# Performance work log

Hardware: AMD Instinct MI355X
Metric: run time of the kernel (lower is better)

The kernel has to match this reference:

```python
import jax, jax.numpy as jnp
import numpy as np

N_LIG, N_TGT, E = 100000, 20000, 1000000
H = 128

def setup_inputs() -> dict:
    key = jax.random.key(0)
    ks = jax.random.split(key, 20)
    def lin(k, fan_in, fan_out):
        k1, k2 = jax.random.split(k)
        lim = 1.0 / np.sqrt(fan_in)
        W = jax.random.uniform(k1, (fan_in, fan_out), jnp.float32, -lim, lim)
        b = jax.random.uniform(k2, (fan_out,), jnp.float32, -lim, lim)
        return W, b
    W_lig, b_lig = lin(ks[0], 4, H)
    W_tgt, b_tgt = lin(ks[1], 1280, H)
    W1f, b1f = lin(ks[2], H, H)   # conv1 ligand->target
    W1r, b1r = lin(ks[3], H, H)   # conv1 target->ligand
    W2f, b2f = lin(ks[4], H, H)   # conv2 ligand->target
    W2r, b2r = lin(ks[5], H, H)   # conv2 target->ligand
    Wp1, bp1 = lin(ks[6], 2 * H, H)  # lin1
    Wp2, bp2 = lin(ks[7], H, 1)      # lin2
    return {
        'x_ligand': jax.random.normal(ks[8], (N_LIG, 4), jnp.float32),
        'x_target': jax.random.normal(ks[9], (N_TGT, 1280), jnp.float32),
        'edge_src': jax.random.randint(ks[10], (E,), 0, N_LIG, jnp.int32),
        'edge_dst': jax.random.randint(ks[11], (E,), 0, N_TGT, jnp.int32),
        'W_lig': W_lig, 'b_lig': b_lig, 'W_tgt': W_tgt, 'b_tgt': b_tgt,
        'W1f': W1f, 'b1f': b1f, 'W1r': W1r, 'b1r': b1r,
        'W2f': W2f, 'b2f': b2f, 'W2r': W2r, 'b2r': b2r,
        'Wp1': Wp1, 'bp1': bp1, 'Wp2': Wp2, 'bp2': bp2,
    }

def _mean_agg(feat, idx, num_segments):
    # scatter-mean: sum / count, 0 for isolated nodes (matches PyG 'mean')
    s = jax.ops.segment_sum(feat, idx, num_segments=num_segments)
    cnt = jax.ops.segment_sum(jnp.ones((idx.shape[0],), feat.dtype), idx,
                              num_segments=num_segments)
    return s / jnp.maximum(cnt, 1.0)[:, None]

def reference(x_ligand, x_target, edge_src, edge_dst,
              W_lig, b_lig, W_tgt, b_tgt,
              W1f, b1f, W1r, b1r, W2f, b2f, W2r, b2r,
              Wp1, bp1, Wp2, bp2):
    h_lig = x_ligand @ W_lig + b_lig   # [N_lig, H]
    h_tgt = x_target @ W_tgt + b_tgt   # [N_tgt, H]

    def conv(h_lig, h_tgt, Wf, bf, Wr, br):
        # ligand -> target (edges as given), target -> ligand (flipped edges)
        agg_t = _mean_agg(h_lig[edge_src], edge_dst, h_tgt.shape[0])
        agg_l = _mean_agg(h_tgt[edge_dst], edge_src, h_lig.shape[0])
        new_tgt = jax.nn.relu(agg_t @ Wf + bf)
        new_lig = jax.nn.relu(agg_l @ Wr + br)
        return new_lig, new_tgt

    h_lig, h_tgt = conv(h_lig, h_tgt, W1f, b1f, W1r, b1r)
    h_lig, h_tgt = conv(h_lig, h_tgt, W2f, b2f, W2r, b2r)

    # per-edge prediction (vectorized gather + tiny MLP), original loops edges
    combined = jnp.concatenate([h_lig[edge_src], h_tgt[edge_dst]], axis=-1)  # [E, 2H]
    pred = jax.nn.relu(combined @ Wp1 + bp1) @ Wp2 + bp2                     # [E, 1]
    return pred
```

## Files before the change

kernel.cpp:

```cpp
#include <hip/hip_runtime.h>
#include <hip/hip_bf16.h>

#define N_LIG 100000
#define N_TGT 20000
#define NEDGE 1000000
#define H 128
#define NXCD 8
#define RL 12500
#define RT 2500
#define CAP 131072
#define NSLICE 16
#define NSLB (NSLICE * NXCD)

typedef __attribute__((ext_vector_type(8))) short short8v;
typedef __attribute__((ext_vector_type(4))) float f32x4;
typedef __attribute__((ext_vector_type(4))) unsigned int uint4v;

__device__ __forceinline__ unsigned short f2bs(float f) {
    unsigned int u = __float_as_uint(f);
    u += 0x7fff + ((u >> 16) & 1);
    return (unsigned short)(u >> 16);
}
__device__ __forceinline__ float bs2f(unsigned int s) {
    return __uint_as_float(s << 16);
}

__global__ void transpose_w(const float* __restrict__ W, unsigned short* __restrict__ Wt, int K) {
    int idx = blockIdx.x * blockDim.x + threadIdx.x;
    if (idx >= K * 128) return;
    int k = idx >> 7, c = idx & 127;
    Wt[(size_t)c * K + k] = f2bs(W[idx]);
}

struct P6 { const float* w[6]; unsigned short* o[6]; };
__global__ void transpose6(P6 p) {
    int idx = blockIdx.x * blockDim.x + threadIdx.x;
    int which = idx >> 14;
    int rem = idx & 16383;
    int k = rem >> 7, c = rem & 127;
    p.o[which][(size_t)c * 128 + k] = f2bs(p.w[which][rem]);
}

__global__ void lin4_bf16(const float* __restrict__ X, const float* __restrict__ W,
                          const float* __restrict__ b, unsigned short* __restrict__ Y, int N) {
    int idx = blockIdx.x * blockDim.x + threadIdx.x;
    if (idx >= N * 16) return;
    int r = idx >> 4;
    int c = (idx & 15) * 8;
    float x0 = X[r * 4 + 0], x1 = X[r * 4 + 1], x2 = X[r * 4 + 2], x3 = X[r * 4 + 3];
    unsigned int o[4];
#pragma unroll
    for (int p = 0; p < 4; ++p) {
        float v0 = b[c + 2 * p] + x0 * W[c + 2 * p] + x1 * W[H + c + 2 * p] +
                   x2 * W[2 * H + c + 2 * p] + x3 * W[3 * H + c + 2 * p];
        float v1 = b[c + 2 * p + 1] + x0 * W[c + 2 * p + 1] + x1 * W[H + c + 2 * p + 1] +
                   x2 * W[2 * H + c + 2 * p + 1] + x3 * W[3 * H + c + 2 * p + 1];
        o[p] = (unsigned int)f2bs(v0) | ((unsigned int)f2bs(v1) << 16);
    }
    uint4 u = make_uint4(o[0], o[1], o[2], o[3]);
    *(uint4*)&Y[(size_t)r * H + c] = u;
}

__launch_bounds__(512)
__global__ void gemm_bf16(const unsigned short* __restrict__ X,
                          const float* __restrict__ Xf32,
                          const unsigned short* __restrict__ Wt,
                          const float* __restrict__ bias,
                          unsigned short* __restrict__ Y,
                          int N, int K, int do_relu) {
    __shared__ unsigned short Ws[128 * 128];
    const int t = threadIdx.x;
    const int wv = t >> 6;
    const int lane = t & 63;
    const int lr = lane & 15;
    const int kb = lane >> 4;
    const int row0 = blockIdx.x * 128;
    const int wrow = wv * 16;

    f32x4 acc[8];
#pragma unroll
    for (int i = 0; i < 8; ++i) acc[i] = (f32x4){0.f, 0.f, 0.f, 0.f};

    int arow = row0 + wrow + lr;
    if (arow >= N) arow = N - 1;
    const unsigned short* xrow = X ? X + (size_t)arow * K : nullptr;
    const float* xrowf = Xf32 ? Xf32 + (size_t)arow * K : nullptr;

    const int nch = K >> 7;
    for (int kc = 0; kc < nch; ++kc) {
        if (kc) __syncthreads();
#pragma unroll
        for (int i = 0; i < 4; ++i) {
            int li = t + i * 512;
            int r = li >> 4;
            int cb = (li & 15) << 4;
            int4 v = *(const int4*)(Wt + (size_t)r * K + (kc << 7) + (cb >> 1));
            *(int4*)((char*)Ws + r * 256 + (cb ^ ((r & 7) << 4))) = v;
        }
        short8v a[4];
        if (xrow) {
#pragma unroll
            for (int ks = 0; ks < 4; ++ks)
                a[ks] = *(const short8v*)(xrow + (kc << 7) + ks * 32 + kb * 8);
        } else {
#pragma unroll
            for (int ks = 0; ks < 4; ++ks) {
                const float* p = xrowf + (kc << 7) + ks * 32 + kb * 8;
                float4 f0 = *(const float4*)p;
                float4 f1 = *(const float4*)(p + 4);
                short8v av;
                av[0] = (short)f2bs(f0.x); av[1] = (short)f2bs(f0.y);
                av[2] = (short)f2bs(f0.z); av[3] = (short)f2bs(f0.w);
                av[4] = (short)f2bs(f1.x); av[5] = (short)f2bs(f1.y);
                av[6] = (short)f2bs(f1.z); av[7] = (short)f2bs(f1.w);
                a[ks] = av;
            }
        }
        __syncthreads();
#pragma unroll
        for (int ks = 0; ks < 4; ++ks) {
            int ofs = ks * 64 + kb * 16;
#pragma unroll
            for (int ct = 0; ct < 8; ++ct) {
                int c = ct * 16 + lr;
                short8v b = *(const short8v*)((const char*)Ws + c * 256 + (ofs ^ ((c & 7) << 4)));
                acc[ct] = __builtin_amdgcn_mfma_f32_16x16x32_bf16(a[ks], b, acc[ct], 0, 0, 0);
            }
        }
    }
    __syncthreads();
#pragma unroll
    for (int ct = 0; ct < 8; ++ct) {
        int col = ct * 16 + lr;
        float bv = bias ? bias[col] : 0.f;
#pragma unroll
        for (int r = 0; r < 4; ++r) {
            float v = acc[ct][r] + bv;
            if (do_relu) v = fmaxf(v, 0.f);
            Ws[(wrow + kb * 4 + r) * 128 + col] = f2bs(v);
        }
    }
    __syncthreads();
#pragma unroll
    for (int i = 0; i < 4; ++i) {
        int li = t + i * 512;
        int r = li >> 4;
        int c8 = (li & 15) << 3;
        int grow = row0 + r;
        if (grow < N)
            *(uint4*)&Y[(size_t)grow * H + c8] = *(const uint4*)&Ws[r * 128 + c8];
    }
}

__global__ void zero_gcur(int* __restrict__ g) {
    if (threadIdx.x < 16) g[threadIdx.x] = 0;
}

__launch_bounds__(256)
__global__ void bin_edges(const int* __restrict__ es, const int* __restrict__ ed,
                          unsigned long long* __restrict__ bkt_l, unsigned int* __restrict__ bkt_t,
                          int* __restrict__ gcur, int E) {
    __shared__ int h[16];
    __shared__ int base_s[16];
    int t = threadIdx.x;
    int lane = t & 63;
    if (t < 16) h[t] = 0;
    __syncthreads();
    int chunk = (E + gridDim.x - 1) / gridDim.x;
    int beg = blockIdx.x * chunk;
    int end = min(beg + chunk, E);
    for (int e0 = beg; e0 < end; e0 += 256) {
        int e = e0 + t;
        int bl = -1, bt = -1;
        if (e < end) { bl = es[e] / RL; bt = ed[e] / RT; }
#pragma unroll
        for (int b = 0; b < 8; ++b) {
            unsigned long long m = __ballot(bl == b);
            if (lane == 0 && m) atomicAdd(&h[b], __popcll(m));
            m = __ballot(bt == b);
            if (lane == 0 && m) atomicAdd(&h[8 + b], __popcll(m));
        }
    }
    __syncthreads();
    if (t < 16) {
        base_s[t] = atomicAdd(&gcur[t], h[t]);
        h[t] = 0;
    }
    __syncthreads();
    for (int e0 = beg; e0 < end; e0 += 256) {
        int e = e0 + t;
        int s = 0, d = 0, bl = -1, bt = -1;
        if (e < end) { s = es[e]; d = ed[e]; bl = s / RL; bt = d / RT; }
        unsigned int low = ((unsigned int)d << 17) | (unsigned int)s;
#pragma unroll
        for (int b = 0; b < 8; ++b) {
            unsigned long long m = __ballot(bl == b);
            if (m) {
                int leader = __ffsll((unsigned long long)m) - 1;
                int rank = __popcll(m & ((1ULL << lane) - 1ULL));
                int wbase = 0;
                if (lane == leader) wbase = atomicAdd(&h[b], __popcll(m));
                wbase = __shfl(wbase, leader);
                if (bl == b) {
                    int i = min(base_s[b] + wbase + rank, CAP - 1);
                    bkt_l[(size_t)b * CAP + i] = ((unsigned long long)(unsigned int)e << 32) | low;
                }
            }
            m = __ballot(bt == b);
            if (m) {
                int leader = __ffsll((unsigned long long)m) - 1;
                int rank = __popcll(m & ((1ULL << lane) - 1ULL));
                int wbase = 0;
                if (lane == leader) wbase = atomicAdd(&h[8 + b], __popcll(m));
                wbase = __shfl(wbase, leader);
                if (bt == b) {
                    int i = min(base_s[8 + b] + wbase + rank, CAP - 1);
                    bkt_t[(size_t)b * CAP + i] = low;
                }
            }
        }
    }
}

__launch_bounds__(256)
__global__ void count_slices(const unsigned long long* __restrict__ bkt_l,
                             const unsigned int* __restrict__ bkt_t,
                             const int* __restrict__ gcur,
                             int* __restrict__ cnts_l, int* __restrict__ cnts_t) {
    __shared__ int h[RL];
    int bi = blockIdx.x;
    int t = threadIdx.x;
    if (bi < NSLB) {
        int p = bi & 7, slice = bi >> 3;
        for (int j = t; j < RL; j += 256) h[j] = 0;
        __syncthreads();
        int n = min(gcur[p], CAP);
        int ss = (n + NSLICE - 1) / NSLICE;
        int beg = slice * ss, end = min(beg + ss, n);
        const unsigned long long* b = bkt_l + (size_t)p * CAP;
        for (int i = beg + t; i < end; i += 256)
            atomicAdd(&h[((unsigned int)b[i] & 0x1FFFF) - p * RL], 1);
        __syncthreads();
        int* dst = cnts_l + (size_t)slice * N_LIG + p * RL;
        for (int j = t; j < RL; j += 256) dst[j] = h[j];
    } else {
        int k = bi - NSLB;
        int p = k & 7, slice = k >> 3;
        for (int j = t; j < RT; j += 256) h[j] = 0;
        __syncthreads();
        int n = min(gcur[8 + p], CAP);
        int ss = (n + NSLICE - 1) / NSLICE;
        int beg = slice * ss, end = min(beg + ss, n);
        const unsigned int* b = bkt_t + (size_t)p * CAP;
        for (int i = beg + t; i < end; i += 256)
            atomicAdd(&h[(int)(b[i] >> 17) - p * RT], 1);
        __syncthreads();
        int* dst = cnts_t + (size_t)slice * N_TGT + p * RT;
        for (int j = t; j < RT; j += 256) dst[j] = h[j];
    }
}

__global__ void scan_block2(int* __restrict__ cnts_l, int* __restrict__ out_l,
                            int* __restrict__ bs_l, int nL, int nbL,
                            int* __restrict__ cnts_t, int* __restrict__ out_t,
                            int* __restrict__ bs_t, int nT) {
    __shared__ int ts[256];
    int* cnts; int* out; int* bsum; int n; int bi; size_t N;
    if ((int)blockIdx.x < nbL) { cnts = cnts_l; out = out_l; bsum = bs_l; n = nL; bi = blockIdx.x; N = N_LIG; }
    else { cnts = cnts_t; out = out_t; bsum = bs_t; n = nT; bi = blockIdx.x - nbL; N = N_TGT; }
    int t = threadIdx.x;
    int base = bi * 1024 + t * 4;
    int v[4] = {0, 0, 0, 0};
    for (int sl = 0; sl < NSLICE; ++sl) {
        size_t o = (size_t)sl * N + base;
#pragma unroll
        for (int i = 0; i < 4; i++) {
            if (base + i < n) {
                int c = cnts[o + i];
                cnts[o + i] = v[i];
                v[i] += c;
            }
        }
    }
    int s = v[0] + v[1] + v[2] + v[3];
    ts[t] = s;
    __syncthreads();
    for (int ofs = 1; ofs < 256; ofs <<= 1) {
        int x = (t >= ofs) ? ts[t - ofs] : 0;
        __syncthreads();
        ts[t] += x;
        __syncthreads();
    }
    int run = (t == 0) ? 0 : ts[t - 1];
    if (t == 255) bsum[bi] = ts[255];
#pragma unroll
    for (int i = 0; i < 4; i++) {
        if (base + i < n) out[base + i] = run;
        run += v[i];
    }
}

__global__ void scan_top2(int* __restrict__ bs_l, int nbL, int* __restrict__ bs_t, int nbT) {
    __shared__ int ts[256];
    int* bsum = (blockIdx.x == 0) ? bs_l : bs_t;
    int nb = (blockIdx.x == 0) ? nbL : nbT;
    int t = threadIdx.x;
    ts[t] = (t < nb) ? bsum[t] : 0;
    __syncthreads();
    for (int ofs = 1; ofs < 256; ofs <<= 1) {
        int x = (t >= ofs) ? ts[t - ofs] : 0;
        __syncthreads();
        ts[t] += x;
        __syncthreads();
    }
    int excl = (t == 0) ? 0 : ts[t - 1];
    if (t < nb) bsum[t] = excl;
}

__global__ void add_off2(int* __restrict__ rp_l, const int* __restrict__ bs_l,
                         int* __restrict__ rp_t, const int* __restrict__ bs_t) {
    int i = blockIdx.x * blockDim.x + threadIdx.x;
    if (i < N_LIG) {
        rp_l[i] += bs_l[i >> 10];
        if (i == 0) rp_l[N_LIG] = NEDGE;
    } else if (i < N_LIG + N_TGT) {
        int j = i - N_LIG;
        rp_t[j] += bs_t[j >> 10];
        if (j == 0) rp_t[N_TGT] = NEDGE;
    }
}

__launch_bounds__(256)
__global__ void fill_slices(const unsigned long long* __restrict__ bkt_l,
                            const unsigned int* __restrict__ bkt_t,
                            const int* __restrict__ gcur,
                            const int* __restrict__ rowptr_l, const int* __restrict__ rowptr_t,
                            const int* __restrict__ cnts_l, const int* __restrict__ cnts_t,
                            int2* __restrict__ elist_l, int* __restrict__ nbr_t) {
    __shared__ int cur[RL];
    int bi = blockIdx.x;
    int t = threadIdx.x;
    if (bi < NSLB) {
        int p = bi & 7, slice = bi >> 3;
        const int* rp = rowptr_l + p * RL;
        const int* pf = cnts_l + (size_t)slice * N_LIG + p * RL;
        for (int j = t; j < RL; j += 256) cur[j] = rp[j] + pf[j];
        __syncthreads();
        int n = min(gcur[p], CAP);
        int ss = (n + NSLICE - 1) / NSLICE;
        int beg = slice * ss, end = min(beg + ss, n);
        const unsigned long long* b = bkt_l + (size_t)p * CAP;
        for (int i = beg + t; i < end; i += 256) {
            unsigned long long v = b[i];
            unsigned int low = (unsigned int)v;
            int pos = atomicAdd(&cur[(low & 0x1FFFF) - p * RL], 1);
            elist_l[pos] = make_int2((int)low, (int)(v >> 32));
        }
    } else {
        int k = bi - NSLB;
        int p = k & 7, slice = k >> 3;
        const int* rp = rowptr_t + p * RT;
        const int* pf = cnts_t + (size_t)slice * N_TGT + p * RT;
        for (int j = t; j < RT; j += 256) cur[j] = rp[j] + pf[j];
        __syncthreads();
        int n = min(gcur[8 + p], CAP);
        int ss = (n + NSLICE - 1) / NSLICE;
        int beg = slice * ss, end = min(beg + ss, n);
        const unsigned int* b = bkt_t + (size_t)p * CAP;
        for (int i = beg + t; i < end; i += 256) {
            unsigned int v = b[i];
            int pos = atomicAdd(&cur[(v >> 17) - p * RT], 1);
            nbr_t[pos] = v & 0x1FFFF;
        }
    }
}

__launch_bounds__(256)
__global__ void gather_g(const unsigned short* __restrict__ feat,
                         const int* __restrict__ rowptr, const int* __restrict__ nbr,
                         int stride, int shr, const float* __restrict__ bias,
                         unsigned short* __restrict__ out, int N) {
    int node = (blockIdx.x * blockDim.x + threadIdx.x) >> 4;
    if (node >= N) return;
    int l16 = threadIdx.x & 15;
    int beg = rowptr[node], end = rowptr[node + 1];
    const uint4v* f4 = (const uint4v*)feat;
    float acc[8] = {0.f, 0.f, 0.f, 0.f, 0.f, 0.f, 0.f, 0.f};
    int j = beg;
    for (; j + 4 <= end; j += 4) {
        unsigned int n0 = ((unsigned int)nbr[(j + 0) * stride]) >> shr;
        unsigned int n1 = ((unsigned int)nbr[(j + 1) * stride]) >> shr;
        unsigned int n2 = ((unsigned int)nbr[(j + 2) * stride]) >> shr;
        unsigned int n3 = ((unsigned int)nbr[(j + 3) * stride]) >> shr;
        uint4v v0 = f4[(size_t)n0 * 16 + l16];
        uint4v v1 = f4[(size_t)n1 * 16 + l16];
        uint4v v2 = f4[(size_t)n2 * 16 + l16];
        uint4v v3 = f4[(size_t)n3 * 16 + l16];
#pragma unroll
        for (int q = 0; q < 4; ++q) {
            acc[2 * q] += (bs2f(v0[q] & 0xffff) + bs2f(v1[q] & 0xffff)) +
                          (bs2f(v2[q] & 0xffff) + bs2f(v3[q] & 0xffff));
            acc[2 * q + 1] += (bs2f(v0[q] >> 16) + bs2f(v1[q] >> 16)) +
                              (bs2f(v2[q] >> 16) + bs2f(v3[q] >> 16));
        }
    }
    for (; j < end; ++j) {
        unsigned int n0 = ((unsigned int)nbr[j * stride]) >> shr;
        uint4v v0 = f4[(size_t)n0 * 16 + l16];
#pragma unroll
        for (int q = 0; q < 4; ++q) {
            acc[2 * q] += bs2f(v0[q] & 0xffff);
            acc[2 * q + 1] += bs2f(v0[q] >> 16);
        }
    }
    float inv = 1.f / (float)max(end - beg, 1);
    uint4v o;
#pragma unroll
    for (int q = 0; q < 4; ++q) {
        float m0 = acc[2 * q] * inv, m1 = acc[2 * q + 1] * inv;
        if (bias) {
            m0 = fmaxf(m0 + bias[l16 * 8 + 2 * q], 0.f);
            m1 = fmaxf(m1 + bias[l16 * 8 + 2 * q + 1], 0.f);
        }
        o[q] = (unsigned int)f2bs(m0) | ((unsigned int)f2bs(m1) << 16);
    }
    ((uint4v*)out)[(size_t)node * 16 + l16] = o;
}

__launch_bounds__(256)
__global__ void edge_mlp_flat(const unsigned short* __restrict__ A16, const unsigned short* __restrict__ B16,
                              const int2* __restrict__ elist,
                              const float* __restrict__ Wp2, const float* __restrict__ bp2,
                              float* __restrict__ out, int E, int ngroups) {
    int gid = (blockIdx.x * blockDim.x + threadIdx.x) >> 4;
    if (gid >= ngroups) return;
    int l16 = threadIdx.x & 15;
    int chunk = (E + ngroups - 1) / ngroups;
    int beg = gid * chunk;
    int end = min(beg + chunk, E);
    if (beg >= end) return;
    float4 w0 = *(const float4*)&Wp2[l16 * 8];
    float4 w1 = *(const float4*)&Wp2[l16 * 8 + 4];
    float wv[8] = {w0.x, w0.y, w0.z, w0.w, w1.x, w1.y, w1.z, w1.w};
    float bp = bp2[0];
    int prev_s = -1;
    float a[8];
    for (int p = beg; p < end; ++p) {
        long long de2 = *(const long long*)&elist[p];
        unsigned int low = (unsigned int)de2;
        int e = (int)(de2 >> 32);
        int s = (int)(low & 0x1FFFF);
        unsigned int d = low >> 17;
        if (s != prev_s) {
            uint4v ua = *(const uint4v*)&A16[(size_t)s * H + l16 * 8];
#pragma unroll
            for (int q = 0; q < 4; ++q) {
                a[2 * q] = bs2f(ua[q] & 0xffff);
                a[2 * q + 1] = bs2f(ua[q] >> 16);
            }
            prev_s = s;
        }
        uint4v ub = *(const uint4v*)&B16[(size_t)d * H + l16 * 8];
        float acc = 0.f;
#pragma unroll
        for (int q = 0; q < 4; ++q) {
            acc += fmaxf(a[2 * q] + bs2f(ub[q] & 0xffff), 0.f) * wv[2 * q];
            acc += fmaxf(a[2 * q + 1] + bs2f(ub[q] >> 16), 0.f) * wv[2 * q + 1];
        }
        acc += __shfl_xor(acc, 8);
        acc += __shfl_xor(acc, 4);
        acc += __shfl_xor(acc, 2);
        acc += __shfl_xor(acc, 1);
        if (l16 == 0) __builtin_nontemporal_store(acc + bp, &out[e]);
    }
}

extern "C" void kernel_launch(void* const* d_in, const int* in_sizes, int n_in,
                              void* d_out, int out_size, void* d_ws, size_t ws_size,
                              hipStream_t stream) {
    const float* x_lig = (const float*)d_in[0];
    const float* x_tgt = (const float*)d_in[1];
    const int* es = (const int*)d_in[2];
    const int* ed = (const int*)d_in[3];
    const float* W_lig = (const float*)d_in[4];
    const float* b_lig = (const float*)d_in[5];
    const float* W_tgt = (const float*)d_in[6];
    const float* b_tgt = (const float*)d_in[7];
    const float* W1f = (const float*)d_in[8];
    const float* b1f = (const float*)d_in[9];
    const float* W1r = (const float*)d_in[10];
    const float* b1r = (const float*)d_in[11];
    const float* W2f = (const float*)d_in[12];
    const float* b2f = (const float*)d_in[13];
    const float* W2r = (const float*)d_in[14];
    const float* b2r = (const float*)d_in[15];
    const float* Wp1 = (const float*)d_in[16];
    const float* bp1 = (const float*)d_in[17];
    const float* Wp2 = (const float*)d_in[18];
    const float* bp2 = (const float*)d_in[19];
    float* out = (float*)d_out;

    char* base = (char*)d_ws;
    size_t off = 0;
    auto alloc = [&](size_t bytes) { char* p = base + off; off = (off + bytes + 255) & ~(size_t)255; return p; };
    unsigned short* L0 = (unsigned short*)alloc((size_t)N_LIG * H * 2);
    unsigned short* L1 = (unsigned short*)alloc((size_t)N_LIG * H * 2);
    unsigned short* T0 = (unsigned short*)alloc((size_t)N_TGT * H * 2);
    unsigned short* T1 = (unsigned short*)alloc((size_t)N_TGT * H * 2);
    unsigned short* G  = (unsigned short*)alloc((size_t)N_TGT * H * 2);
    unsigned short* Wt_tgt = (unsigned short*)alloc((size_t)128 * 1280 * 2);
    unsigned short* Wt1f = (unsigned short*)alloc(128 * 128 * 2);
    unsigned short* Wt1r = (unsigned short*)alloc(128 * 128 * 2);
    unsigned short* Wt2f = (unsigned short*)alloc(128 * 128 * 2);
    unsigned short* Wt2r = (unsigned short*)alloc(128 * 128 * 2);
    unsigned short* WtA = (unsigned short*)alloc(128 * 128 * 2);
    unsigned short* WtB = (unsigned short*)alloc(128 * 128 * 2);
    int* cnts_l = (int*)alloc((size_t)NSLICE * N_LIG * 4);
    int* cnts_t = (int*)alloc((size_t)NSLICE * N_TGT * 4);
    int* rowptr_l = (int*)alloc((N_LIG + 4) * 4);
    int* rowptr_t = (int*)alloc((N_TGT + 4) * 4);
    int* bsum_l = (int*)alloc(256 * 4);
    int* bsum_t = (int*)alloc(256 * 4);
    int* gcur = (int*)alloc(16 * 4);
    int2* elist_l = (int2*)alloc((size_t)NEDGE * 8);
    int* nbr_t = (int*)alloc((size_t)NEDGE * 4);
    unsigned long long* bkt_l = (unsigned long long*)alloc((size_t)NXCD * CAP * 8);
    unsigned int* bkt_t = (unsigned int*)alloc((size_t)NXCD * CAP * 4);

    const int ligBlocks = (N_LIG + 127) / 128;
    const int tgtBlocks = (N_TGT + 127) / 128;
    const int nbL = (N_LIG + 1023) / 1024;
    const int nbT = (N_TGT + 1023) / 1024;

    transpose_w<<<(1280 * 128 + 255) / 256, 256, 0, stream>>>(W_tgt, Wt_tgt, 1280);
    P6 p6;
    p6.w[0] = W1f; p6.o[0] = Wt1f;
    p6.w[1] = W1r; p6.o[1] = Wt1r;
    p6.w[2] = W2f; p6.o[2] = Wt2f;
    p6.w[3] = W2r; p6.o[3] = Wt2r;
    p6.w[4] = Wp1;           p6.o[4] = WtA;
    p6.w[5] = Wp1 + 128 * H; p6.o[5] = WtB;
    transpose6<<<6 * 64, 256, 0, stream>>>(p6);

    lin4_bf16<<<(N_LIG * 16 + 255) / 256, 256, 0, stream>>>(x_lig, W_lig, b_lig, L0, N_LIG);
    gemm_bf16<<<tgtBlocks, 512, 0, stream>>>(nullptr, x_tgt, Wt_tgt, b_tgt, T0, N_TGT, 1280, 0);

    zero_gcur<<<1, 64, 0, stream>>>(gcur);
    bin_edges<<<512, 256, 0, stream>>>(es, ed, bkt_l, bkt_t, gcur, NEDGE);
    count_slices<<<2 * NSLB, 256, 0, stream>>>(bkt_l, bkt_t, gcur, cnts_l, cnts_t);
    scan_block2<<<nbL + nbT, 256, 0, stream>>>(cnts_l, rowptr_l, bsum_l, N_LIG, nbL,
                                               cnts_t, rowptr_t, bsum_t, N_TGT);
    scan_top2<<<2, 256, 0, stream>>>(bsum_l, nbL, bsum_t, nbT);
    add_off2<<<(N_LIG + N_TGT + 255) / 256, 256, 0, stream>>>(rowptr_l, bsum_l, rowptr_t, bsum_t);
    fill_slices<<<2 * NSLB, 256, 0, stream>>>(bkt_l, bkt_t, gcur, rowptr_l, rowptr_t,
                                              cnts_l, cnts_t, elist_l, nbr_t);

    const unsigned short* Wtf[2] = {Wt1f, Wt2f};
    const float* bfp[2] = {b1f, b2f};
    const unsigned short* Wtr[2] = {Wt1r, Wt2r};
    const float* brp[2] = {b1r, b2r};
    unsigned short* Lcur = L0;
    unsigned short* Lnxt = L1;
    for (int layer = 0; layer < 2; ++layer) {
        gemm_bf16<<<tgtBlocks, 512, 0, stream>>>(T0, nullptr, Wtr[layer], nullptr, G, N_TGT, 128, 0);
        gather_g<<<(int)(((size_t)N_TGT * 16 + 255) / 256), 256, 0, stream>>>(
            Lcur, rowptr_t, nbr_t, 1, 0, nullptr, T1, N_TGT);
        gather_g<<<(int)(((size_t)N_LIG * 16 + 255) / 256), 256, 0, stream>>>(
            G, rowptr_l, (const int*)elist_l, 2, 17, brp[layer], Lnxt, N_LIG);
        gemm_bf16<<<tgtBlocks, 512, 0, stream>>>(T1, nullptr, Wtf[layer], bfp[layer], T0, N_TGT, 128, 1);
        unsigned short* tmp = Lcur; Lcur = Lnxt; Lnxt = tmp;
    }

    gemm_bf16<<<ligBlocks, 512, 0, stream>>>(L0, nullptr, WtA, nullptr, L1, N_LIG, 128, 0);
    gemm_bf16<<<tgtBlocks, 512, 0, stream>>>(T0, nullptr, WtB, bp1, T1, N_TGT, 128, 0);

    const int ngroups = 32768;
    edge_mlp_flat<<<ngroups / 16, 256, 0, stream>>>(
        L1, T1, elist_l, Wp2, bp2, out, NEDGE, ngroups);
}
```

Baseline: 374.8 us.

## Read GEMM weights directly from global memory and use per-wave epilogue staging

The bf16 GEMM no longer stages the weight tile in shared memory. Each wave now loads its B fragments straight from global memory, which should hit in cache, and this removes all block-wide barriers. The epilogue stages results in a per-wave LDS buffer, so no block barrier is needed there either. Optionally, non-temporal stores are used for the large ligand projection output. The trade-off is many more global and L1 loads of the weights per wave, including redundant reads across the 8 waves, in exchange for dropping LDS staging and synchronisation.

Result: slower. 478.9 us (+27.8%).

```diff
diff --git a/kernel.cpp b/kernel.cpp
--- a/kernel.cpp
+++ b/kernel.cpp
@@ -67,8 +67,8 @@
                           const unsigned short* __restrict__ Wt,
                           const float* __restrict__ bias,
                           unsigned short* __restrict__ Y,
-                          int N, int K, int do_relu) {
-    __shared__ unsigned short Ws[128 * 128];
+                          int N, int K, int do_relu, int nt) {
+    __shared__ unsigned short Es[8][16][128];
     const int t = threadIdx.x;
     const int wv = t >> 6;
     const int lane = t & 63;
@@ -88,15 +88,6 @@
 
     const int nch = K >> 7;
     for (int kc = 0; kc < nch; ++kc) {
-        if (kc) __syncthreads();
-#pragma unroll
-        for (int i = 0; i < 4; ++i) {
-            int li = t + i * 512;
-            int r = li >> 4;
-            int cb = (li & 15) << 4;
-            int4 v = *(const int4*)(Wt + (size_t)r * K + (kc << 7) + (cb >> 1));
-            *(int4*)((char*)Ws + r * 256 + (cb ^ ((r & 7) << 4))) = v;
-        }
         short8v a[4];
         if (xrow) {
 #pragma unroll
@@ -116,19 +107,16 @@
                 a[ks] = av;
             }
         }
-        __syncthreads();
 #pragma unroll
         for (int ks = 0; ks < 4; ++ks) {
-            int ofs = ks * 64 + kb * 16;
 #pragma unroll
             for (int ct = 0; ct < 8; ++ct) {
                 int c = ct * 16 + lr;
-                short8v b = *(const short8v*)((const char*)Ws + c * 256 + (ofs ^ ((c & 7) << 4)));
+                short8v b = *(const short8v*)(Wt + (size_t)c * K + (kc << 7) + ks * 32 + kb * 8);
                 acc[ct] = __builtin_amdgcn_mfma_f32_16x16x32_bf16(a[ks], b, acc[ct], 0, 0, 0);
             }
         }
     }
-    __syncthreads();
 #pragma unroll
     for (int ct = 0; ct < 8; ++ct) {
         int col = ct * 16 + lr;
@@ -137,18 +125,20 @@
         for (int r = 0; r < 4; ++r) {
             float v = acc[ct][r] + bv;
             if (do_relu) v = fmaxf(v, 0.f);
-            Ws[(wrow + kb * 4 + r) * 128 + col] = f2bs(v);
-        }
-    }
-    __syncthreads();
+            Es[wv][kb * 4 + r][col] = f2bs(v);
+        }
+    }
 #pragma unroll
     for (int i = 0; i < 4; ++i) {
-        int li = t + i * 512;
+        int li = lane + i * 64;
         int r = li >> 4;
         int c8 = (li & 15) << 3;
-        int grow = row0 + r;
-        if (grow < N)
-            *(uint4*)&Y[(size_t)grow * H + c8] = *(const uint4*)&Ws[r * 128 + c8];
+        int grow = row0 + wrow + r;
+        if (grow < N) {
+            uint4v v = *(const uint4v*)&Es[wv][r][c8];
+            if (nt) __builtin_nontemporal_store(v, (uint4v*)&Y[(size_t)grow * H + c8]);
+            else    *(uint4v*)&Y[(size_t)grow * H + c8] = v;
+        }
     }
 }
 
@@ -543,7 +533,7 @@
     transpose6<<<6 * 64, 256, 0, stream>>>(p6);
 
     lin4_bf16<<<(N_LIG * 16 + 255) / 256, 256, 0, stream>>>(x_lig, W_lig, b_lig, L0, N_LIG);
-    gemm_bf16<<<tgtBlocks, 512, 0, stream>>>(nullptr, x_tgt, Wt_tgt, b_tgt, T0, N_TGT, 1280, 0);
+    gemm_bf16<<<tgtBlocks, 512, 0, stream>>>(nullptr, x_tgt, Wt_tgt, b_tgt, T0, N_TGT, 1280, 0, 0);
 
     zero_gcur<<<1, 64, 0, stream>>>(gcur);
     bin_edges<<<512, 256, 0, stream>>>(es, ed, bkt_l, bkt_t, gcur, NEDGE);
@@ -562,17 +552,17 @@
     unsigned short* Lcur = L0;
     unsigned short* Lnxt = L1;
     for (int layer = 0; layer < 2; ++layer) {
-        gemm_bf16<<<tgtBlocks, 512, 0, stream>>>(T0, nullptr, Wtr[layer], nullptr, G, N_TGT, 128, 0);
+        gemm_bf16<<<tgtBlocks, 512, 0, stream>>>(T0, nullptr, Wtr[layer], nullptr, G, N_TGT, 128, 0, 0);
         gather_g<<<(int)(((size_t)N_TGT * 16 + 255) / 256), 256, 0, stream>>>(
             Lcur, rowptr_t, nbr_t, 1, 0, nullptr, T1, N_TGT);
         gather_g<<<(int)(((size_t)N_LIG * 16 + 255) / 256), 256, 0, stream>>>(
             G, rowptr_l, (const int*)elist_l, 2, 17, brp[layer], Lnxt, N_LIG);
-        gemm_bf16<<<tgtBlocks, 512, 0, stream>>>(T1, nullptr, Wtf[layer], bfp[layer], T0, N_TGT, 128, 1);
+        gemm_bf16<<<tgtBlocks, 512, 0, stream>>>(T1, nullptr, Wtf[layer], bfp[layer], T0, N_TGT, 128, 1, 0);
         unsigned short* tmp = Lcur; Lcur = Lnxt; Lnxt = tmp;
     }
 
-    gemm_bf16<<<ligBlocks, 512, 0, stream>>>(L0, nullptr, WtA, nullptr, L1, N_LIG, 128, 0);
-    gemm_bf16<<<tgtBlocks, 512, 0, stream>>>(T0, nullptr, WtB, bp1, T1, N_TGT, 128, 0);
+    gemm_bf16<<<ligBlocks, 512, 0, stream>>>(L0, nullptr, WtA, nullptr, L1, N_LIG, 128, 0, 1);
+    gemm_bf16<<<tgtBlocks, 512, 0, stream>>>(T0, nullptr, WtB, bp1, T1, N_TGT, 128, 0, 0);
 
     const int ngroups = 32768;
     edge_mlp_flat<<<ngroups / 16, 256, 0, stream>>>(
```
